# Optimization experiments

Measured on AMD Instinct MI355X. Metric: run time of the kernel, lower is better.

Reference implementation:

```python
import jax, jax.numpy as jnp
import numpy as np

B, S, D, H = 2, 2048, 1024, 16
DK = D // H

def setup_inputs() -> dict:
    key = jax.random.key(0)
    k_x, k_q, k_k, k_v, k_o = jax.random.split(key, 5)
    return {
        "x": jax.random.normal(k_x, (B, S, D), dtype=jnp.float32),
        "wq": jax.random.normal(k_q, (D, D), dtype=jnp.float32) * 0.02,
        "wk": jax.random.normal(k_k, (D, D), dtype=jnp.float32) * 0.02,
        "wv": jax.random.normal(k_v, (D, D), dtype=jnp.float32) * 0.02,
        "wo": jax.random.normal(k_o, (D, D), dtype=jnp.float32) * 0.02,
    }

def reference(x, wq, wk, wv, wo):
    b, s, d = x.shape
    # project and split heads: [b, h, s, dk]
    q = (x @ wq).reshape(b, s, H, DK).transpose(0, 2, 1, 3)
    k = (x @ wk).reshape(b, s, H, DK).transpose(0, 2, 1, 3)
    v = (x @ wv).reshape(b, s, H, DK).transpose(0, 2, 1, 3)
    scores = jnp.einsum("bhqd,bhkd->bhqk", q, k) / jnp.sqrt(jnp.float32(DK))
    causal = jnp.tril(jnp.ones((s, s), dtype=bool))  # True = keep
    scores = jnp.where(causal, scores, jnp.finfo(scores.dtype).min)
    probs = jax.nn.softmax(scores, axis=-1)  # dropout pdrop=0.0 -> identity
    out = jnp.einsum("bhqk,bhkd->bhqd", probs, v)
    out = out.transpose(0, 2, 1, 3).reshape(b, s, d)
    return out @ wo
```

## Files before the change

### kernel.cpp

```cpp
#include <hip/hip_runtime.h>
#include <hip/hip_bf16.h>

typedef short s16x8 __attribute__((ext_vector_type(8)));
typedef float f32x4 __attribute__((ext_vector_type(4)));
typedef float f32x16 __attribute__((ext_vector_type(16)));
typedef unsigned short u16x4 __attribute__((ext_vector_type(4)));
typedef unsigned int u32x4 __attribute__((ext_vector_type(4)));

#define D_MODEL 1024
#define N_HEAD  16
#define D_HEAD  64
#define SEQ     2048
#define NBATCH  2

#if __has_builtin(__builtin_amdgcn_exp2f)
#define EXP2(x) __builtin_amdgcn_exp2f(x)
#else
#define EXP2(x) exp2f(x)
#endif

#define GLOAD_LDS16(g, l) \
    __builtin_amdgcn_global_load_lds((const __attribute__((address_space(1))) void*)(g), \
                                     (__attribute__((address_space(3))) void*)(l), 16, 0, 0)

__device__ __forceinline__ unsigned short f2bf(float f) {
    union { float f; unsigned int u; } v; v.f = f;
    unsigned int r = v.u + 0x7FFFu + ((v.u >> 16) & 1u);
    return (unsigned short)(r >> 16);
}

__device__ __forceinline__ unsigned cvtpk_bf16(float lo, float hi) {
    unsigned r;
    asm("v_cvt_pk_bf16_f32 %0, %1, %2" : "=v"(r) : "v"(lo), "v"(hi));
    return r;
}


__global__ __launch_bounds__(256) void cvt_x_kernel(const float* __restrict__ in,
                                                    unsigned short* __restrict__ out) {
    int i = (blockIdx.x * 256 + threadIdx.x) * 4;
    float4 v = *reinterpret_cast<const float4*>(in + i);
    u16x4 o;
    o.x = f2bf(v.x); o.y = f2bf(v.y); o.z = f2bf(v.z); o.w = f2bf(v.w);
    *reinterpret_cast<u16x4*>(out + i) = o;
}

__global__ __launch_bounds__(256) void cvt_w_kernel(
    const float* __restrict__ w0, const float* __restrict__ w1,
    const float* __restrict__ w2, const float* __restrict__ w3,
    unsigned short* __restrict__ o0, unsigned short* __restrict__ o1,
    unsigned short* __restrict__ o2, unsigned short* __restrict__ o3)
{
    __shared__ unsigned short T[64][72];
    const int t = threadIdx.x;
    const int z = blockIdx.y;
    const float* w = (z == 0) ? w0 : (z == 1) ? w1 : (z == 2) ? w2 : w3;
    unsigned short* wt = (z == 0) ? o0 : (z == 1) ? o1 : (z == 2) ? o2 : o3;
    const int k0 = ((int)blockIdx.x & 15) * 64, n0 = ((int)blockIdx.x >> 4) * 64;
#pragma unroll
    for (int i = 0; i < 4; ++i) {
        int k = (t >> 4) + i * 16;
        int n = (t & 15) * 4;
        float4 v = *reinterpret_cast<const float4*>(&w[(k0 + k) * 1024 + n0 + n]);
        T[n + 0][k] = f2bf(v.x); T[n + 1][k] = f2bf(v.y);
        T[n + 2][k] = f2bf(v.z); T[n + 3][k] = f2bf(v.w);
    }
    __syncthreads();
#pragma unroll
    for (int i = 0; i < 2; ++i) {
        int n = (t >> 3) + i * 32;
        int kc = (t & 7) * 8;
        *reinterpret_cast<s16x8*>(&wt[(n0 + n) * 1024 + k0 + kc]) =
            *reinterpret_cast<const s16x8*>(&T[n][kc]);
    }
}


__global__ __launch_bounds__(256, 3) void gemm_qkv_kernel(
    const unsigned short* __restrict__ xb,
    const unsigned short* __restrict__ wqt, const unsigned short* __restrict__ wkt,
    const unsigned short* __restrict__ wvt,
    unsigned short* __restrict__ Qb, unsigned short* __restrict__ Kb,
    unsigned short* __restrict__ Vtb)
{
    __shared__ unsigned short As[128 * 64];
    __shared__ unsigned short Bs[128 * 64];
    const int t = threadIdx.x, lane = t & 63, wid = t >> 6;
    const int wr = wid >> 1, wc = wid & 1;
    const int l15 = lane & 15, l4 = lane >> 4;
    const int m0 = blockIdx.y * 128, n0 = blockIdx.x * 128;
    const int z = blockIdx.z;
    const unsigned short* Bt = (z == 0) ? wqt : (z == 1) ? wkt : wvt;

    const int srow = t >> 3;
    const int srcoff = (((t & 7) ^ (srow & 7)) << 3);
    const unsigned short* Ab = xb + (size_t)(m0 + srow) * D_MODEL + srcoff;
    const unsigned short* Bb = Bt + (size_t)(n0 + srow) * D_MODEL + srcoff;
    const int ldsoff = t * 8;
    const int rsw = l15 & 7;

    f32x4 acc[4][4];
#pragma unroll
    for (int m = 0; m < 4; ++m)
#pragma unroll
        for (int n = 0; n < 4; ++n) acc[m][n] = (f32x4){0.f, 0.f, 0.f, 0.f};

    for (int k0 = 0; k0 < D_MODEL; k0 += 64) {
        __syncthreads();
#pragma unroll
        for (int i = 0; i < 4; ++i) {
            GLOAD_LDS16(Ab + (size_t)(i * 32) * D_MODEL + k0, &As[i * 2048 + ldsoff]);
            GLOAD_LDS16(Bb + (size_t)(i * 32) * D_MODEL + k0, &Bs[i * 2048 + ldsoff]);
        }
        __syncthreads();

#pragma unroll
        for (int ks = 0; ks < 2; ++ks) {
            const int csl = ks * 4 + l4;
            s16x8 af[4], bfr[4];
#pragma unroll
            for (int m = 0; m < 4; ++m)
                af[m] = *reinterpret_cast<const s16x8*>(
                    &As[(wr * 64 + m * 16 + l15) * 64 + ((csl ^ rsw) << 3)]);
#pragma unroll
            for (int n = 0; n < 4; ++n)
                bfr[n] = *reinterpret_cast<const s16x8*>(
                    &Bs[(wc * 64 + n * 16 + l15) * 64 + ((csl ^ rsw) << 3)]);
            __builtin_amdgcn_s_setprio(1);
#pragma unroll
            for (int m = 0; m < 4; ++m)
#pragma unroll
                for (int n = 0; n < 4; ++n)
                    acc[m][n] = __builtin_amdgcn_mfma_f32_16x16x32_bf16(af[m], bfr[n], acc[m][n], 0, 0, 0);
            __builtin_amdgcn_s_setprio(0);
        }
    }

    const int rb = m0 + wr * 64, cb = n0 + wc * 64;
    if (z == 2) {
#pragma unroll
        for (int m = 0; m < 4; ++m) {
            int row = rb + m * 16 + l4 * 4;
            int b = row >> 11, s = row & 2047;
#pragma unroll
            for (int n = 0; n < 4; ++n) {
                int col = cb + n * 16 + l15;
                int h = col >> 6, dk = col & 63;
                u16x4 o;
                o.x = f2bf(acc[m][n][0]); o.y = f2bf(acc[m][n][1]);
                o.z = f2bf(acc[m][n][2]); o.w = f2bf(acc[m][n][3]);
                *reinterpret_cast<u16x4*>(&Vtb[(((b * N_HEAD + h) * D_HEAD + dk) << 11) + s]) = o;
            }
        }
    } else {
        unsigned short* C = (z == 0) ? Qb : Kb;
        const float alpha = (z == 0) ? 0.18033688011112042f : 1.0f;
#pragma unroll
        for (int m = 0; m < 4; ++m)
#pragma unroll
            for (int n = 0; n < 4; ++n)
#pragma unroll
                for (int r = 0; r < 4; ++r)
                    C[(rb + m * 16 + l4 * 4 + r) * D_MODEL + cb + n * 16 + l15] =
                        f2bf(acc[m][n][r] * alpha);
    }
}


__global__ __launch_bounds__(256, 3) void gemm_out_kernel(
    const unsigned short* __restrict__ attnb, const unsigned short* __restrict__ wot,
    float* __restrict__ out)
{
    __shared__ unsigned short As[128 * 64];
    __shared__ unsigned short Bs[64 * 64];
    const int t = threadIdx.x, lane = t & 63, wid = t >> 6;
    const int wr = wid >> 1, wc = wid & 1;
    const int l15 = lane & 15, l4 = lane >> 4;
    const int m0 = blockIdx.y * 128, n0 = blockIdx.x * 64;

    const int srow = t >> 3;
    const int srcoff = (((t & 7) ^ (srow & 7)) << 3);
    const unsigned short* Ab = attnb + (size_t)(m0 + srow) * D_MODEL + srcoff;
    const unsigned short* Bb = wot + (size_t)(n0 + srow) * D_MODEL + srcoff;
    const int ldsoff = t * 8;
    const int rsw = l15 & 7;

    f32x4 acc[4][2];
#pragma unroll
    for (int m = 0; m < 4; ++m)
#pragma unroll
        for (int n = 0; n < 2; ++n) acc[m][n] = (f32x4){0.f, 0.f, 0.f, 0.f};

    for (int k0 = 0; k0 < D_MODEL; k0 += 64) {
        __syncthreads();
#pragma unroll
        for (int i = 0; i < 4; ++i)
            GLOAD_LDS16(Ab + (size_t)(i * 32) * D_MODEL + k0, &As[i * 2048 + ldsoff]);
#pragma unroll
        for (int i = 0; i < 2; ++i)
            GLOAD_LDS16(Bb + (size_t)(i * 32) * D_MODEL + k0, &Bs[i * 2048 + ldsoff]);
        __syncthreads();

#pragma unroll
        for (int ks = 0; ks < 2; ++ks) {
            const int csl = ks * 4 + l4;
            s16x8 af[4], bfr[2];
#pragma unroll
            for (int m = 0; m < 4; ++m)
                af[m] = *reinterpret_cast<const s16x8*>(
                    &As[(wr * 64 + m * 16 + l15) * 64 + ((csl ^ rsw) << 3)]);
#pragma unroll
            for (int n = 0; n < 2; ++n)
                bfr[n] = *reinterpret_cast<const s16x8*>(
                    &Bs[(wc * 32 + n * 16 + l15) * 64 + ((csl ^ rsw) << 3)]);
            __builtin_amdgcn_s_setprio(1);
#pragma unroll
            for (int m = 0; m < 4; ++m)
#pragma unroll
                for (int n = 0; n < 2; ++n)
                    acc[m][n] = __builtin_amdgcn_mfma_f32_16x16x32_bf16(af[m], bfr[n], acc[m][n], 0, 0, 0);
            __builtin_amdgcn_s_setprio(0);
        }
    }

    const int rb = m0 + wr * 64, cb = n0 + wc * 32;
#pragma unroll
    for (int m = 0; m < 4; ++m)
#pragma unroll
        for (int n = 0; n < 2; ++n)
#pragma unroll
            for (int r = 0; r < 4; ++r)
                out[(rb + m * 16 + l4 * 4 + r) * D_MODEL + cb + n * 16 + l15] = acc[m][n][r];
}


__global__ __launch_bounds__(512, 2) void attn_kernel(
    const unsigned short* __restrict__ Qb, const unsigned short* __restrict__ Kb,
    const unsigned short* __restrict__ Vtb, unsigned short* __restrict__ Ob)
{
    __shared__ unsigned short SMEM[16384];

    const int t = threadIdx.x;
    const int lane = t & 63, wid = t >> 6;
    const int l31 = lane & 31, l5 = lane >> 5;
    const int bh = blockIdx.y, b = bh >> 4, h = bh & 15;
    const int q0 = ((int)gridDim.x - 1 - (int)blockIdx.x) * 256;
    const int qw = q0 + wid * 32;
    const int qrow = qw + l31;

    s16x8 qf[4];
#pragma unroll
    for (int ks = 0; ks < 4; ++ks)
        qf[ks] = *reinterpret_cast<const s16x8*>(
            &Qb[(size_t)(b * SEQ + qrow) * D_MODEL + h * D_HEAD + ks * 16 + l5 * 8]);

    f32x16 oacc[2];
#pragma unroll
    for (int d = 0; d < 2; ++d)
#pragma unroll
        for (int r = 0; r < 16; ++r) oacc[d][r] = 0.f;
    float lrun = 0.f;

    const int wk = wid & 3;
    const int srow = lane >> 3;
    const int scol = ((lane & 7) ^ srow) * 8;
    const unsigned short* kgb = Kb + (size_t)(b * SEQ + wk * 16 + srow) * D_MODEL + h * D_HEAD + scol;
    const unsigned short* vgb = Vtb + ((size_t)(bh * D_HEAD + wk * 16 + srow) << 11) + scol;
    const int swz = (l31 & 7);

#define STAGE(bufidx, kvbase) do { \
    if (wid < 4) { \
        const unsigned short* kg = kgb + (size_t)(kvbase) * D_MODEL; \
        GLOAD_LDS16(kg,                         &SMEM[(bufidx) * 4096 + (wk * 16) * 64]); \
        GLOAD_LDS16(kg + (size_t)8 * D_MODEL,   &SMEM[(bufidx) * 4096 + (wk * 16 + 8) * 64]); \
    } else { \
        const unsigned short* vg = vgb + (kvbase); \
        GLOAD_LDS16(vg,                         &SMEM[8192 + (bufidx) * 4096 + (wk * 16) * 64]); \
        GLOAD_LDS16(vg + ((size_t)8 << 11),     &SMEM[8192 + (bufidx) * 4096 + (wk * 16 + 8) * 64]); \
    } } while (0)

    const int ntiles = (q0 >> 6) + 4;
    STAGE(0, 0);

    for (int ti = 0; ti < ntiles; ++ti) {
        const int cur = ti & 1;
        const int kv0 = ti * 64;
        __builtin_amdgcn_sched_barrier(0);
        asm volatile("s_waitcnt vmcnt(0)" ::: "memory");
        __builtin_amdgcn_s_barrier();
        if (ti + 1 < ntiles) STAGE(cur ^ 1, kv0 + 64);
        __builtin_amdgcn_sched_barrier(0);

        if (kv0 > qw + 31) continue;

        const unsigned short* KsC = &SMEM[cur * 4096];
        const unsigned short* VsC = &SMEM[8192 + cur * 4096];

        f32x16 sacc[2];
#pragma unroll
        for (int kvsub = 0; kvsub < 2; ++kvsub) {
            const bool active = (kv0 + kvsub * 32 <= qw + 31);
            if (active) {
#pragma unroll
                for (int r = 0; r < 16; ++r) sacc[kvsub][r] = -8.0f;
                __builtin_amdgcn_s_setprio(1);
#pragma unroll
                for (int ks = 0; ks < 4; ++ks) {
                    s16x8 kf = *reinterpret_cast<const s16x8*>(
                        &KsC[(kvsub * 32 + l31) * 64 + (((2 * ks + l5) ^ swz) * 8)]);
                    sacc[kvsub] = __builtin_amdgcn_mfma_f32_32x32x16_bf16(kf, qf[ks], sacc[kvsub], 0, 0, 0);
                }
                __builtin_amdgcn_s_setprio(0);
                if (kv0 + kvsub * 32 + 31 > qw) {
                    int kvbase = kv0 + kvsub * 32 + 4 * l5;
#pragma unroll
                    for (int r = 0; r < 16; ++r) {
                        int kvg = kvbase + (r & 3) + 8 * (r >> 2);
                        sacc[kvsub][r] = (kvg > qrow) ? -1e30f : sacc[kvsub][r];
                    }
                }
#pragma unroll
                for (int r = 0; r < 16; ++r) sacc[kvsub][r] = EXP2(sacc[kvsub][r]);
            } else {
#pragma unroll
                for (int r = 0; r < 16; ++r) sacc[kvsub][r] = 0.f;
            }
        }

        float sred[16];
#pragma unroll
        for (int r = 0; r < 16; ++r) sred[r] = sacc[0][r] + sacc[1][r];
#pragma unroll
        for (int s = 8; s >= 1; s >>= 1)
#pragma unroll
            for (int r = 0; r < 8; ++r)
                if (r < s) sred[r] += sred[r + s];
        lrun += sred[0] + __shfl_xor(sred[0], 32);

#pragma unroll
        for (int ks = 0; ks < 4; ++ks) {
            if (kv0 + (ks >> 1) * 32 > qw + 31) continue;
            const int kvsub = ks >> 1, bo = (ks & 1) * 8;
            unsigned a0 = cvtpk_bf16(sacc[kvsub][bo + 0], sacc[kvsub][bo + 1]);
            unsigned a1 = cvtpk_bf16(sacc[kvsub][bo + 2], sacc[kvsub][bo + 3]);
            unsigned a2 = cvtpk_bf16(sacc[kvsub][bo + 4], sacc[kvsub][bo + 5]);
            unsigned a3 = cvtpk_bf16(sacc[kvsub][bo + 6], sacc[kvsub][bo + 7]);
            asm volatile("v_permlane32_swap_b32 %0, %1" : "+v"(a0), "+v"(a2));
            asm volatile("v_permlane32_swap_b32 %0, %1" : "+v"(a1), "+v"(a3));
            u32x4 pw; pw.x = a0; pw.y = a1; pw.z = a2; pw.w = a3;
            s16x8 pf = __builtin_bit_cast(s16x8, pw);
            __builtin_amdgcn_s_setprio(1);
#pragma unroll
            for (int dsub = 0; dsub < 2; ++dsub) {
                s16x8 vf = *reinterpret_cast<const s16x8*>(
                    &VsC[(dsub * 32 + l31) * 64 + (((2 * ks + l5) ^ swz) * 8)]);
                oacc[dsub] = __builtin_amdgcn_mfma_f32_32x32x16_bf16(vf, pf, oacc[dsub], 0, 0, 0);
            }
            __builtin_amdgcn_s_setprio(0);
        }
    }
    __syncthreads();

    float inv = 1.f / lrun;
    const int orow = wid * 32 + l31;
#pragma unroll
    for (int dsub = 0; dsub < 2; ++dsub)
#pragma unroll
        for (int a = 0; a < 4; ++a) {
            unsigned w0 = cvtpk_bf16(oacc[dsub][4 * a + 0] * inv, oacc[dsub][4 * a + 1] * inv);
            unsigned w1 = cvtpk_bf16(oacc[dsub][4 * a + 2] * inv, oacc[dsub][4 * a + 3] * inv);
            int slot = (4 * dsub + a) ^ (orow & 7);
            uint2 pr; pr.x = w0; pr.y = w1;
            *reinterpret_cast<uint2*>(&SMEM[orow * 64 + slot * 8 + l5 * 4]) = pr;
        }
    __syncthreads();
#pragma unroll
    for (int i = 0; i < 4; ++i) {
        int s = i * 512 + t;
        int row = s >> 3, c16 = s & 7;
        int cs = (c16 ^ (row & 7)) * 8;
        s16x8 v = *reinterpret_cast<const s16x8*>(&SMEM[row * 64 + cs]);
        *reinterpret_cast<s16x8*>(
            &Ob[(size_t)(b * SEQ + q0 + row) * D_MODEL + h * D_HEAD + c16 * 8]) = v;
    }
#undef STAGE
}


extern "C" void kernel_launch(void* const* d_in, const int* in_sizes, int n_in,
                              void* d_out, int out_size, void* d_ws, size_t ws_size,
                              hipStream_t stream) {
    (void)in_sizes; (void)n_in; (void)out_size; (void)ws_size;
    const float* x  = (const float*)d_in[0];
    const float* wq = (const float*)d_in[1];
    const float* wk = (const float*)d_in[2];
    const float* wv = (const float*)d_in[3];
    const float* wo = (const float*)d_in[4];
    float* out = (float*)d_out;

    char* ws = (char*)d_ws;
    unsigned short* xb  = (unsigned short*)(ws);
    unsigned short* wqt = (unsigned short*)(ws + (8u  << 20));
    unsigned short* wkt = (unsigned short*)(ws + (10u << 20));
    unsigned short* wvt = (unsigned short*)(ws + (12u << 20));
    unsigned short* wot = (unsigned short*)(ws + (14u << 20));
    unsigned short* Qb  = (unsigned short*)(ws + (16u << 20));
    unsigned short* Kb  = (unsigned short*)(ws + (24u << 20));
    unsigned short* Vtb = (unsigned short*)(ws + (32u << 20));
    unsigned short* Ob  = (unsigned short*)(ws + (40u << 20));

    hipLaunchKernelGGL(cvt_x_kernel, dim3(4096), dim3(256), 0, stream, x, xb);
    hipLaunchKernelGGL(cvt_w_kernel, dim3(256, 4), dim3(256), 0, stream,
                       wq, wk, wv, wo, wqt, wkt, wvt, wot);

    hipLaunchKernelGGL(gemm_qkv_kernel, dim3(8, 32, 3), dim3(256), 0, stream,
                       xb, wqt, wkt, wvt, Qb, Kb, Vtb);
    hipLaunchKernelGGL(attn_kernel, dim3(8, 32), dim3(512), 0, stream, Qb, Kb, Vtb, Ob);
    hipLaunchKernelGGL(gemm_out_kernel, dim3(16, 32), dim3(256), 0, stream, Ob, wot, out);
}
```

Baseline: 110.0 us.

## Split long causal attention rows across two blocks and merge with combine kernel

Attention blocks shrink to 128 query rows and 256 threads. For the longer causal rows (upper half of the sequence) the KV range is split between two blocks that write unnormalized bf16 partial outputs and row sums into reused workspace. A new combine kernel then adds the two partials and normalizes them. The goal is to even out the causal work imbalance and raise occupancy, at the cost of an extra launch, extra global traffic, and extra bf16 rounding of the partials. Because a fixed max of 8 is used instead of a running max, the partials can be added directly without rescaling.

```diff
diff --git a/kernel.cpp b/kernel.cpp
--- a/kernel.cpp
+++ b/kernel.cpp
@@ -27,6 +27,11 @@
     union { float f; unsigned int u; } v; v.f = f;
     unsigned int r = v.u + 0x7FFFu + ((v.u >> 16) & 1u);
     return (unsigned short)(r >> 16);
+}
+
+__device__ __forceinline__ float bf2f(unsigned short u) {
+    union { unsigned int u; float f; } v; v.u = ((unsigned int)u) << 16;
+    return v.f;
 }
 
 __device__ __forceinline__ unsigned cvtpk_bf16(float lo, float hi) {
@@ -234,17 +239,36 @@
 }
 
 
-__global__ __launch_bounds__(512, 2) void attn_kernel(
+__global__ __launch_bounds__(256, 4) void attn_kernel(
     const unsigned short* __restrict__ Qb, const unsigned short* __restrict__ Kb,
-    const unsigned short* __restrict__ Vtb, unsigned short* __restrict__ Ob)
+    const unsigned short* __restrict__ Vtb, unsigned short* __restrict__ Ob,
+    unsigned short* __restrict__ Opart, float* __restrict__ larr)
 {
-    __shared__ unsigned short SMEM[16384];
+    __shared__ unsigned short SMEM[8192];
+    __shared__ unsigned short SMEMV[8192];
 
     const int t = threadIdx.x;
     const int lane = t & 63, wid = t >> 6;
     const int l31 = lane & 31, l5 = lane >> 5;
-    const int bh = blockIdx.y, b = bh >> 4, h = bh & 15;
-    const int q0 = ((int)gridDim.x - 1 - (int)blockIdx.x) * 256;
+
+    const int bid = blockIdx.x;
+    int bh, s, ta, tb; bool split;
+    if (bid < 512) {
+        bh = bid >> 4;
+        int r = bid & 15;
+        s = 8 + (r >> 1);
+        int c = r & 1;
+        int half = s + 1;
+        ta = c * half; tb = ta + half;
+        split = true;
+    } else {
+        int u = bid - 512;
+        bh = u >> 3; s = u & 7;
+        ta = 0; tb = 2 * (s + 1);
+        split = false;
+    }
+    const int b = bh >> 4, h = bh & 15;
+    const int q0 = s << 7;
     const int qw = q0 + wid * 32;
     const int qrow = qw + l31;
 
@@ -261,40 +285,41 @@
         for (int r = 0; r < 16; ++r) oacc[d][r] = 0.f;
     float lrun = 0.f;
 
-    const int wk = wid & 3;
+    const int stK = (wid & 1) * 32;
     const int srow = lane >> 3;
     const int scol = ((lane & 7) ^ srow) * 8;
-    const unsigned short* kgb = Kb + (size_t)(b * SEQ + wk * 16 + srow) * D_MODEL + h * D_HEAD + scol;
-    const unsigned short* vgb = Vtb + ((size_t)(bh * D_HEAD + wk * 16 + srow) << 11) + scol;
+    const unsigned short* kgb = Kb + (size_t)(b * SEQ + stK + srow) * D_MODEL + h * D_HEAD + scol;
+    const unsigned short* vgb = Vtb + ((size_t)(bh * D_HEAD + stK + srow) << 11) + scol;
     const int swz = (l31 & 7);
 
 #define STAGE(bufidx, kvbase) do { \
-    if (wid < 4) { \
+    if (wid < 2) { \
         const unsigned short* kg = kgb + (size_t)(kvbase) * D_MODEL; \
-        GLOAD_LDS16(kg,                         &SMEM[(bufidx) * 4096 + (wk * 16) * 64]); \
-        GLOAD_LDS16(kg + (size_t)8 * D_MODEL,   &SMEM[(bufidx) * 4096 + (wk * 16 + 8) * 64]); \
+        _Pragma("unroll") \
+        for (int i_ = 0; i_ < 4; ++i_) \
+            GLOAD_LDS16(kg + (size_t)(i_ * 8) * D_MODEL, &SMEM[(bufidx) * 4096 + (stK + i_ * 8) * 64]); \
     } else { \
         const unsigned short* vg = vgb + (kvbase); \
-        GLOAD_LDS16(vg,                         &SMEM[8192 + (bufidx) * 4096 + (wk * 16) * 64]); \
-        GLOAD_LDS16(vg + ((size_t)8 << 11),     &SMEM[8192 + (bufidx) * 4096 + (wk * 16 + 8) * 64]); \
+        _Pragma("unroll") \
+        for (int i_ = 0; i_ < 4; ++i_) \
+            GLOAD_LDS16(vg + ((size_t)(i_ * 8) << 11), &SMEMV[(bufidx) * 4096 + (stK + i_ * 8) * 64]); \
     } } while (0)
 
-    const int ntiles = (q0 >> 6) + 4;
-    STAGE(0, 0);
-
-    for (int ti = 0; ti < ntiles; ++ti) {
-        const int cur = ti & 1;
+    STAGE(0, ta * 64);
+
+    for (int ti = ta; ti < tb; ++ti) {
+        const int cur = (ti - ta) & 1;
         const int kv0 = ti * 64;
         __builtin_amdgcn_sched_barrier(0);
         asm volatile("s_waitcnt vmcnt(0)" ::: "memory");
         __builtin_amdgcn_s_barrier();
-        if (ti + 1 < ntiles) STAGE(cur ^ 1, kv0 + 64);
+        if (ti + 1 < tb) STAGE(cur ^ 1, (ti + 1) * 64);
         __builtin_amdgcn_sched_barrier(0);
 
         if (kv0 > qw + 31) continue;
 
         const unsigned short* KsC = &SMEM[cur * 4096];
-        const unsigned short* VsC = &SMEM[8192 + cur * 4096];
+        const unsigned short* VsC = &SMEMV[cur * 4096];
 
         f32x16 sacc[2];
 #pragma unroll
@@ -331,10 +356,10 @@
 #pragma unroll
         for (int r = 0; r < 16; ++r) sred[r] = sacc[0][r] + sacc[1][r];
 #pragma unroll
-        for (int s = 8; s >= 1; s >>= 1)
+        for (int sj = 8; sj >= 1; sj >>= 1)
 #pragma unroll
             for (int r = 0; r < 8; ++r)
-                if (r < s) sred[r] += sred[r + s];
+                if (r < sj) sred[r] += sred[r + sj];
         lrun += sred[0] + __shfl_xor(sred[0], 32);
 
 #pragma unroll
@@ -361,7 +386,7 @@
     }
     __syncthreads();
 
-    float inv = 1.f / lrun;
+    float inv = split ? 1.0f : (1.0f / lrun);
     const int orow = wid * 32 + l31;
 #pragma unroll
     for (int dsub = 0; dsub < 2; ++dsub)
@@ -374,16 +399,57 @@
             *reinterpret_cast<uint2*>(&SMEM[orow * 64 + slot * 8 + l5 * 4]) = pr;
         }
     __syncthreads();
+    if (split) {
+        unsigned short* Op = Opart + (size_t)bid * 8192;
+#pragma unroll
+        for (int i = 0; i < 4; ++i) {
+            int g = i * 256 + t;
+            int row = g >> 3, c16 = g & 7;
+            int cs = (c16 ^ (row & 7)) * 8;
+            *reinterpret_cast<s16x8*>(&Op[row * 64 + c16 * 8]) =
+                *reinterpret_cast<const s16x8*>(&SMEM[row * 64 + cs]);
+        }
+        if (l5 == 0) larr[bid * 128 + orow] = lrun;
+    } else {
+#pragma unroll
+        for (int i = 0; i < 4; ++i) {
+            int g = i * 256 + t;
+            int row = g >> 3, c16 = g & 7;
+            int cs = (c16 ^ (row & 7)) * 8;
+            s16x8 v = *reinterpret_cast<const s16x8*>(&SMEM[row * 64 + cs]);
+            *reinterpret_cast<s16x8*>(
+                &Ob[(size_t)(b * SEQ + q0 + row) * D_MODEL + h * D_HEAD + c16 * 8]) = v;
+        }
+    }
+#undef STAGE
+}
+
+
+__global__ __launch_bounds__(256) void combine_kernel(
+    const unsigned short* __restrict__ Opart, const float* __restrict__ larr,
+    unsigned short* __restrict__ Ob)
+{
+    const int u = blockIdx.x;
+    const int bh = u >> 3, s = (u & 7) + 8;
+    const int b = bh >> 4, h = bh & 15;
+    const int slotA = u * 2, slotB = slotA + 1;
+    const unsigned short* A = Opart + (size_t)slotA * 8192;
+    const unsigned short* B = Opart + (size_t)slotB * 8192;
+    const int t = threadIdx.x;
 #pragma unroll
     for (int i = 0; i < 4; ++i) {
-        int s = i * 512 + t;
-        int row = s >> 3, c16 = s & 7;
-        int cs = (c16 ^ (row & 7)) * 8;
-        s16x8 v = *reinterpret_cast<const s16x8*>(&SMEM[row * 64 + cs]);
+        int g = i * 256 + t;
+        int row = g >> 3, c8 = (g & 7) * 8;
+        float inv = 1.0f / (larr[slotA * 128 + row] + larr[slotB * 128 + row]);
+        s16x8 va = *reinterpret_cast<const s16x8*>(&A[row * 64 + c8]);
+        s16x8 vb = *reinterpret_cast<const s16x8*>(&B[row * 64 + c8]);
+        union { s16x8 v; unsigned short e[8]; } o;
+#pragma unroll
+        for (int j = 0; j < 8; ++j)
+            o.e[j] = f2bf((bf2f((unsigned short)va[j]) + bf2f((unsigned short)vb[j])) * inv);
         *reinterpret_cast<s16x8*>(
-            &Ob[(size_t)(b * SEQ + q0 + row) * D_MODEL + h * D_HEAD + c16 * 8]) = v;
-    }
-#undef STAGE
+            &Ob[(size_t)(b * SEQ + s * 128 + row) * D_MODEL + h * D_HEAD + c8]) = o.v;
+    }
 }
 
 
@@ -408,6 +474,8 @@
     unsigned short* Kb  = (unsigned short*)(ws + (24u << 20));
     unsigned short* Vtb = (unsigned short*)(ws + (32u << 20));
     unsigned short* Ob  = (unsigned short*)(ws + (40u << 20));
+    unsigned short* Opart = xb;
+    float*          larr  = (float*)wqt;
 
     hipLaunchKernelGGL(cvt_x_kernel, dim3(4096), dim3(256), 0, stream, x, xb);
     hipLaunchKernelGGL(cvt_w_kernel, dim3(256, 4), dim3(256), 0, stream,
@@ -415,6 +483,8 @@
 
     hipLaunchKernelGGL(gemm_qkv_kernel, dim3(8, 32, 3), dim3(256), 0, stream,
                        xb, wqt, wkt, wvt, Qb, Kb, Vtb);
-    hipLaunchKernelGGL(attn_kernel, dim3(8, 32), dim3(512), 0, stream, Qb, Kb, Vtb, Ob);
+    hipLaunchKernelGGL(attn_kernel, dim3(768), dim3(256), 0, stream,
+                       Qb, Kb, Vtb, Ob, Opart, larr);
+    hipLaunchKernelGGL(combine_kernel, dim3(256), dim3(256), 0, stream, Opart, larr, Ob);
     hipLaunchKernelGGL(gemm_out_kernel, dim3(16, 32), dim3(256), 0, stream, Ob, wot, out);
 }
```

New measurement: 102.4 us. 6.9% less time.
